# Kernel tuning notes

Hardware: AMD Instinct MI355X
Metric: run time of the kernel (lower is better)

## Reference

```python
import jax, jax.numpy as jnp
import numpy as np

N_NODES = 100000


def gcn_conv(x, src, dst, W, b, n):
    # PyG GCNConv: h = x @ W; add self-loops; sym-normalize; scatter-add; + bias
    h = x @ W                                        # [N, out]
    loop = jnp.arange(n, dtype=src.dtype)
    src2 = jnp.concatenate([src, loop])              # [E+N]
    dst2 = jnp.concatenate([dst, loop])
    deg = jax.ops.segment_sum(jnp.ones_like(dst2, dtype=h.dtype), dst2, num_segments=n)
    dis = jnp.where(deg > 0, jax.lax.rsqrt(deg), 0.0)
    norm = dis[src2] * dis[dst2]                     # [E+N]
    msg = h[src2] * norm[:, None]                    # gather + scale
    out = jax.ops.segment_sum(msg, dst2, num_segments=n)  # scatter-add
    return out + b


def setup_inputs() -> dict:
    key = jax.random.key(0)
    ks = jax.random.split(key, 8)
    F_in, H = 128, 64
    E = 1200000
    x = jax.random.normal(ks[0], (N_NODES, F_in), dtype=jnp.float32)
    edge_index = jax.random.randint(ks[1], (2, E), 0, N_NODES, dtype=jnp.int64)
    s = 1.0 / np.sqrt(F_in)
    W1 = jax.random.normal(ks[2], (F_in, H), dtype=jnp.float32) * s
    b1 = jnp.zeros((H,), dtype=jnp.float32)
    W2 = jax.random.normal(ks[3], (H, H), dtype=jnp.float32) * (1.0 / np.sqrt(H))
    b2 = jnp.zeros((H,), dtype=jnp.float32)
    W3 = jax.random.normal(ks[4], (H, 1), dtype=jnp.float32) * (1.0 / np.sqrt(H))
    b3 = jnp.zeros((1,), dtype=jnp.float32)
    return {"x": x, "edge_index": edge_index, "W1": W1, "b1": b1,
            "W2": W2, "b2": b2, "W3": W3, "b3": b3}


def reference(x, edge_index, W1, b1, W2, b2, W3, b3):
    n = x.shape[0]
    src, dst = edge_index[0], edge_index[1]
    h = jax.nn.relu(gcn_conv(x, src, dst, W1, b1, n))
    h = jax.nn.relu(gcn_conv(h, src, dst, W2, b2, n))
    return (h @ W3 + b3)[:, 0]  # squeeze(-1) -> [N]
```

## Files before the change

### kernel.cpp

```cpp
#include <hip/hip_runtime.h>

#define NF 64
#define NBKMAX 512
#define CHUNK 4096
#define CAP   4096

typedef __attribute__((ext_vector_type(8))) short bf16x8;
typedef __attribute__((ext_vector_type(4))) float f32x4;

__device__ __forceinline__ unsigned short f2bf(float f) {
    union { float f; unsigned u; } c; c.f = f;
    unsigned u = c.u;
    return (unsigned short)((u + 0x7FFFu + ((u >> 16) & 1u)) >> 16);
}
__device__ __forceinline__ float bf2f1(unsigned short v) {
    union { unsigned u; float f; } c; c.u = ((unsigned)v) << 16;
    return c.f;
}
__device__ __forceinline__ float2 bfp2(unsigned v) {
    union { unsigned u; float f; } lo, hi;
    lo.u = v << 16;
    hi.u = v & 0xffff0000u;
    return make_float2(lo.f, hi.f);
}

__global__ __launch_bounds__(256) void k_prep(int* __restrict__ bcnt, int nbk,
                                              const float* __restrict__ W1,
                                              unsigned short* __restrict__ wt1h,
                                              unsigned short* __restrict__ wt1l,
                                              const float* __restrict__ W2,
                                              unsigned short* __restrict__ wt2h,
                                              unsigned short* __restrict__ wt2l) {
    int idx = blockIdx.x * 256 + threadIdx.x;
    if (idx < 512) {
        if (idx < nbk) bcnt[idx] = 0;
    } else if (idx < 512 + 128 * 64) {
        int e = idx - 512;
        int k = e >> 6, col = e & 63;
        float w = W1[e];
        unsigned short h = f2bf(w);
        wt1h[col * 128 + k] = h;
        wt1l[col * 128 + k] = f2bf(w - bf2f1(h));
    } else if (idx < 512 + 128 * 64 + 64 * 64) {
        int e = idx - 512 - 128 * 64;
        int k = e >> 6, col = e & 63;
        float w = W2[e];
        unsigned short h = f2bf(w);
        wt2h[col * 64 + k] = h;
        wt2l[col * 64 + k] = f2bf(w - bf2f1(h));
    }
}

__device__ __forceinline__ void load8f(const float* A, bool ok, size_t off, float* v) {
    if (ok) {
        float4 a = *(const float4*)&A[off];
        float4 b = *(const float4*)&A[off + 4];
        v[0]=a.x; v[1]=a.y; v[2]=a.z; v[3]=a.w;
        v[4]=b.x; v[5]=b.y; v[6]=b.z; v[7]=b.w;
    } else { for (int j = 0; j < 8; ++j) v[j] = 0.f; }
}
__device__ __forceinline__ void load8f(const unsigned short* A, bool ok, size_t off, float* v) {
    if (ok) {
        uint4 u = *(const uint4*)&A[off];
        float2 p0 = bfp2(u.x), p1 = bfp2(u.y), p2 = bfp2(u.z), p3 = bfp2(u.w);
        v[0]=p0.x; v[1]=p0.y; v[2]=p1.x; v[3]=p1.y;
        v[4]=p2.x; v[5]=p2.y; v[6]=p3.x; v[7]=p3.y;
    } else { for (int j = 0; j < 8; ++j) v[j] = 0.f; }
}

template<int K>
__device__ __forceinline__ void stage_w(const unsigned short* __restrict__ Wt_hi_g,
                                        const unsigned short* __restrict__ Wt_lo_g,
                                        unsigned short* __restrict__ sWh,
                                        unsigned short* __restrict__ sWl, int tid) {
    constexpr int KS = K / 8, SM = KS - 1;
    for (int idx = tid; idx < 64 * KS; idx += 256) {
        int col = idx / KS, slot = idx % KS;
        int d = col * K + 8 * (slot ^ (col & SM));
        *(uint4*)&sWh[d] = *(const uint4*)&Wt_hi_g[col * K + slot * 8];
        *(uint4*)&sWl[d] = *(const uint4*)&Wt_lo_g[col * K + slot * 8];
    }
}

template<int K, bool HASBIAS, typename AT>
__device__ __forceinline__ void gemm_core(const AT* __restrict__ A,
                                          const unsigned short* __restrict__ sWh,
                                          const unsigned short* __restrict__ sWl,
                                          const float* __restrict__ bias_in,
                                          unsigned short* __restrict__ out,
                                          int n, int rb, int tid) {
    constexpr int KS = K / 8, SM = KS - 1, NS = K / 32;
    const int w = tid >> 6, l = tid & 63;
    const int lr = l & 15, lg = l >> 4;
    const int arow = rb + w * 16 + lr;
    const bool ok = arow < n;

    float v[NS][8];
    #pragma unroll
    for (int s = 0; s < NS; ++s)
        load8f(A, ok, (size_t)arow * K + s * 32 + lg * 8, v[s]);

    f32x4 acc[4] = {};
    #pragma unroll
    for (int s = 0; s < NS; ++s) {
        if (HASBIAS) {
            #pragma unroll
            for (int j = 0; j < 8; ++j)
                v[s][j] = fmaxf(v[s][j] + bias_in[s * 32 + lg * 8 + j], 0.f);
        }
        unsigned short h8[8], l8[8];
        #pragma unroll
        for (int j = 0; j < 8; ++j) {
            h8[j] = f2bf(v[s][j]);
            l8[j] = f2bf(v[s][j] - bf2f1(h8[j]));
        }
        const bf16x8 ah = *(const bf16x8*)h8;
        const bf16x8 al = *(const bf16x8*)l8;
        #pragma unroll
        for (int ct = 0; ct < 4; ++ct) {
            int col  = ct * 16 + lr;
            int boff = col * K + 8 * ((s * 4 + lg) ^ (col & SM));
            const bf16x8 bh = *(const bf16x8*)&sWh[boff];
            const bf16x8 bl = *(const bf16x8*)&sWl[boff];
            acc[ct] = __builtin_amdgcn_mfma_f32_16x16x32_bf16(ah, bh, acc[ct], 0, 0, 0);
            acc[ct] = __builtin_amdgcn_mfma_f32_16x16x32_bf16(ah, bl, acc[ct], 0, 0, 0);
            acc[ct] = __builtin_amdgcn_mfma_f32_16x16x32_bf16(al, bh, acc[ct], 0, 0, 0);
        }
    }

    #pragma unroll
    for (int i = 0; i < 4; ++i) {
        int r = rb + w * 16 + lg * 4 + i;
        if (r < n) {
            #pragma unroll
            for (int ct = 0; ct < 4; ++ct)
                out[(size_t)r * NF + ct * 16 + lr] = f2bf(acc[ct][i]);
        }
    }
}

struct ScatS {
    unsigned stage[CHUNK];
    unsigned short stb[CHUNK];
    int hist[NBKMAX];
    int base[NBKMAX];
};
struct GemmS {
    unsigned short sWh[64 * 128];
    unsigned short sWl[64 * 128];
};
union USmem { ScatS s; GemmS g; };

__global__ __launch_bounds__(256) void k_scat_gemm(
        const int* __restrict__ src, const int* __restrict__ dst,
        int* __restrict__ bcnt, unsigned* __restrict__ pairs4, int E, int nbk, int nscat,
        const float* __restrict__ A,
        const unsigned short* __restrict__ Wt_hi_g, const unsigned short* __restrict__ Wt_lo_g,
        unsigned short* __restrict__ out, int n) {
    __shared__ USmem u;
    const int tid = threadIdx.x;

    if ((int)blockIdx.x < nscat) {
        int e0 = blockIdx.x * CHUNK;
        int cnt = E - e0; if (cnt > CHUNK) cnt = CHUNK;
        for (int i = tid; i < nbk; i += 256) u.s.hist[i] = 0;
        __syncthreads();
        for (int i = tid; i < cnt; i += 256) {
            int s = src[e0 + i], d = dst[e0 + i];
            u.s.stage[i] = ((unsigned)s << 8) | ((unsigned)d & 255u);
            u.s.stb[i]   = (unsigned short)(((unsigned)d) >> 8);
            atomicAdd(&u.s.hist[((unsigned)d) >> 8], 1);
        }
        __syncthreads();
        for (int i = tid; i < nbk; i += 256) {
            int c = u.s.hist[i];
            u.s.base[i] = c ? atomicAdd(&bcnt[i], c) : 0;
            u.s.hist[i] = 0;
        }
        __syncthreads();
        for (int i = tid; i < cnt; i += 256) {
            int b = u.s.stb[i];
            int off = u.s.base[b] + atomicAdd(&u.s.hist[b], 1);
            if (off < CAP) pairs4[(size_t)b * CAP + off] = u.s.stage[i];
        }
        return;
    }

    const int rb = ((int)blockIdx.x - nscat) * 64;
    stage_w<128>(Wt_hi_g, Wt_lo_g, u.g.sWh, u.g.sWl, tid);
    __syncthreads();
    gemm_core<128, false>(A, u.g.sWh, u.g.sWl, nullptr, out, n, rb, tid);
}

__global__ __launch_bounds__(256) void k_bsort2(const unsigned* __restrict__ pairs4,
                                                const int* __restrict__ bcnt,
                                                int* __restrict__ start, int* __restrict__ endp,
                                                int* __restrict__ adj,
                                                float* __restrict__ dis, int n) {
    __shared__ int cnt[256];
    __shared__ int cur[256];
    int b   = blockIdx.x;
    int nb  = b << 8;
    int nn  = n - nb; if (nn > 256) nn = 256;
    int ec  = bcnt[b]; if (ec > CAP) ec = CAP;
    int pbI = b * CAP;
    size_t pb = (size_t)pbI;
    int t = threadIdx.x;
    cnt[t] = 0;
    __syncthreads();
    for (int i = t; i < ec; i += 256)
        atomicAdd(&cnt[pairs4[pb + i] & 255u], 1);
    __syncthreads();
    int v = cnt[t];
    __syncthreads();
    for (int off = 1; off < 256; off <<= 1) {
        int u = (t >= off) ? cnt[t - off] : 0;
        __syncthreads();
        cnt[t] += u;
        __syncthreads();
    }
    int exc = cnt[t] - v;
    if (t < nn) {
        start[nb + t] = pbI + exc;
        endp[nb + t]  = pbI + exc + v;
        dis[nb + t]   = rsqrtf((float)(v + 1));
    }
    cur[t] = exc;
    __syncthreads();
    for (int i = t; i < ec; i += 256) {
        unsigned p = pairs4[pb + i];
        int off = atomicAdd(&cur[p & 255u], 1);
        adj[pbI + off] = (int)(p >> 8);
    }
}

__global__ __launch_bounds__(256) void k_mgemm64(const unsigned short* __restrict__ A,
                                                 const unsigned short* __restrict__ Wt_hi_g,
                                                 const unsigned short* __restrict__ Wt_lo_g,
                                                 const float* __restrict__ bias_in,
                                                 unsigned short* __restrict__ out, int n) {
    __shared__ unsigned short sWh[64 * 64];
    __shared__ unsigned short sWl[64 * 64];
    const int tid = threadIdx.x;
    const int rb = blockIdx.x * 64;
    stage_w<64>(Wt_hi_g, Wt_lo_g, sWh, sWl, tid);
    __syncthreads();
    gemm_core<64, true>(A, sWh, sWl, bias_in, out, n, rb, tid);
}

__global__ __launch_bounds__(256) void k_gather(const unsigned short* __restrict__ g,
                                                const int* __restrict__ adj,
                                                const int* __restrict__ start,
                                                const int* __restrict__ endp,
                                                const float* __restrict__ dis,
                                                unsigned short* __restrict__ agg, int n) {
    int node = blockIdx.x * 16 + (threadIdx.x >> 4);
    int fl   = threadIdx.x & 15;
    int gb   = threadIdx.x & 48;
    if (node >= n) return;
    int s = start[node], e = endp[node];
    float dn = dis[node];
    uint2 v = *(const uint2*)&g[(size_t)node * NF + fl * 4];
    float2 pa = bfp2(v.x), pb = bfp2(v.y);
    float4 acc = make_float4(pa.x * dn, pa.y * dn, pb.x * dn, pb.y * dn);
    for (int base = s; base < e; base += 16) {
        int m = e - base; if (m > 16) m = 16;
        int idx = (fl < m) ? adj[base + fl] : 0;
        for (int j = 0; j < m; ++j) {
            int u = __shfl(idx, gb + j);
            float du = dis[u];
            uint2 w = *(const uint2*)&g[(size_t)u * NF + fl * 4];
            float2 q0 = bfp2(w.x), q1 = bfp2(w.y);
            acc.x += q0.x * du; acc.y += q0.y * du;
            acc.z += q1.x * du; acc.w += q1.y * du;
        }
    }
    ushort4 o;
    o.x = f2bf(acc.x * dn);
    o.y = f2bf(acc.y * dn);
    o.z = f2bf(acc.z * dn);
    o.w = f2bf(acc.w * dn);
    *(ushort4*)&agg[(size_t)node * NF + fl * 4] = o;
}

__global__ __launch_bounds__(256) void k_gather_final(const unsigned short* __restrict__ g,
                                                      const int* __restrict__ adj,
                                                      const int* __restrict__ start,
                                                      const int* __restrict__ endp,
                                                      const float* __restrict__ dis,
                                                      const float* __restrict__ b2,
                                                      const float* __restrict__ W3,
                                                      const float* __restrict__ b3,
                                                      float* __restrict__ out, int n) {
    int node = blockIdx.x * 16 + (threadIdx.x >> 4);
    int fl   = threadIdx.x & 15;
    int gb   = threadIdx.x & 48;
    if (node >= n) return;
    int s = start[node], e = endp[node];
    float dn = dis[node];
    uint2 v = *(const uint2*)&g[(size_t)node * NF + fl * 4];
    float2 pa = bfp2(v.x), pb = bfp2(v.y);
    float4 acc = make_float4(pa.x * dn, pa.y * dn, pb.x * dn, pb.y * dn);
    for (int base = s; base < e; base += 16) {
        int m = e - base; if (m > 16) m = 16;
        int idx = (fl < m) ? adj[base + fl] : 0;
        for (int j = 0; j < m; ++j) {
            int u = __shfl(idx, gb + j);
            float du = dis[u];
            uint2 w = *(const uint2*)&g[(size_t)u * NF + fl * 4];
            float2 q0 = bfp2(w.x), q1 = bfp2(w.y);
            acc.x += q0.x * du; acc.y += q0.y * du;
            acc.z += q1.x * du; acc.w += q1.y * du;
        }
    }
    const float4 bb = *(const float4*)&b2[fl * 4];
    const float4 ww = *(const float4*)&W3[fl * 4];
    float r = fmaxf(acc.x * dn + bb.x, 0.f) * ww.x
            + fmaxf(acc.y * dn + bb.y, 0.f) * ww.y
            + fmaxf(acc.z * dn + bb.z, 0.f) * ww.z
            + fmaxf(acc.w * dn + bb.w, 0.f) * ww.w;
    #pragma unroll
    for (int off = 8; off > 0; off >>= 1) r += __shfl_down(r, off, 16);
    if (fl == 0) out[node] = r + b3[0];
}

extern "C" void kernel_launch(void* const* d_in, const int* in_sizes, int n_in,
                              void* d_out, int out_size, void* d_ws, size_t ws_size,
                              hipStream_t stream) {
    const float* x  = (const float*)d_in[0];
    const int*   ei = (const int*)d_in[1];
    const float* W1 = (const float*)d_in[2];
    const float* b1 = (const float*)d_in[3];
    const float* W2 = (const float*)d_in[4];
    const float* b2 = (const float*)d_in[5];
    const float* W3 = (const float*)d_in[6];
    const float* b3 = (const float*)d_in[7];
    float* out = (float*)d_out;

    const int n = out_size;
    const int E = in_sizes[1] / 2;
    const int* src = ei;
    const int* dst = ei + E;
    const int ns  = (n + 255) & ~255;
    const int nbk = (n + 255) >> 8;

    char* w = (char*)d_ws;
    float* dis   = (float*)w;  w += (size_t)ns * 4;
    int*   start = (int*)w;    w += (size_t)ns * 4;
    int*   endp  = (int*)w;    w += (size_t)ns * 4;
    int*   adj   = (int*)w;    w += (size_t)nbk * CAP * 4;
    int*   bcnt  = (int*)w;    w += NBKMAX * 4;
    unsigned short* wt1h = (unsigned short*)w;  w += 64 * 128 * 2;
    unsigned short* wt1l = (unsigned short*)w;  w += 64 * 128 * 2;
    unsigned short* wt2h = (unsigned short*)w;  w += 64 * 64 * 2;
    unsigned short* wt2l = (unsigned short*)w;  w += 64 * 64 * 2;
    unsigned short* gbuf1 = (unsigned short*)w;  w += (size_t)n * NF * 2;
    unsigned short* gbuf2 = (unsigned short*)w;  w += (size_t)n * NF * 2;
    unsigned short* aggb  = (unsigned short*)w;  w += (size_t)n * NF * 2;
    unsigned* pairs4 = (unsigned*)w;

    const int B = 256;
    const int nscat = (E + CHUNK - 1) / CHUNK;
    const int ngemm = (n + 63) / 64;

    k_prep<<<(512 + 128 * 64 + 64 * 64 + B - 1) / B, B, 0, stream>>>(
        bcnt, nbk, W1, wt1h, wt1l, W2, wt2h, wt2l);
    k_scat_gemm<<<nscat + ngemm, B, 0, stream>>>(
        src, dst, bcnt, pairs4, E, nbk, nscat, x, wt1h, wt1l, gbuf1, n);
    k_bsort2<<<nbk, B, 0, stream>>>(pairs4, bcnt, start, endp, adj, dis, n);

    k_gather<<<(n + 15) / 16, B, 0, stream>>>(gbuf1, adj, start, endp, dis, aggb, n);

    k_mgemm64<<<ngemm, B, 0, stream>>>(aggb, wt2h, wt2l, b1, gbuf2, n);
    k_gather_final<<<(n + 15) / 16, B, 0, stream>>>(gbuf2, adj, start, endp, dis, b2, W3, b3, out, n);
}
```

Before: 128.4 us.

## Fuse layer-1 neighbor gather with layer-2 GEMM via shared memory

Merges the first-layer aggregation kernel and the second-layer 64x64 GEMM into one 1024-thread kernel. Each block gathers 64 nodes into fp32 shared memory, then applies bias, ReLU and the split-bf16 MFMA GEMM straight from LDS. This removes the aggb intermediate round trip through global memory and one kernel launch. In exchange, the large 1024-thread blocks may reduce occupancy and stall on the slowest node's gather, and the gathered values skip the bf16 rounding they had before.

Result: slower. 134.3 us (+4.6%).

```diff
diff --git a/kernel.cpp b/kernel.cpp
--- a/kernel.cpp
+++ b/kernel.cpp
@@ -59,83 +59,18 @@
         v[4]=b.x; v[5]=b.y; v[6]=b.z; v[7]=b.w;
     } else { for (int j = 0; j < 8; ++j) v[j] = 0.f; }
 }
-__device__ __forceinline__ void load8f(const unsigned short* A, bool ok, size_t off, float* v) {
-    if (ok) {
-        uint4 u = *(const uint4*)&A[off];
-        float2 p0 = bfp2(u.x), p1 = bfp2(u.y), p2 = bfp2(u.z), p3 = bfp2(u.w);
-        v[0]=p0.x; v[1]=p0.y; v[2]=p1.x; v[3]=p1.y;
-        v[4]=p2.x; v[5]=p2.y; v[6]=p3.x; v[7]=p3.y;
-    } else { for (int j = 0; j < 8; ++j) v[j] = 0.f; }
-}
 
 template<int K>
 __device__ __forceinline__ void stage_w(const unsigned short* __restrict__ Wt_hi_g,
                                         const unsigned short* __restrict__ Wt_lo_g,
                                         unsigned short* __restrict__ sWh,
-                                        unsigned short* __restrict__ sWl, int tid) {
+                                        unsigned short* __restrict__ sWl, int tid, int nthr) {
     constexpr int KS = K / 8, SM = KS - 1;
-    for (int idx = tid; idx < 64 * KS; idx += 256) {
+    for (int idx = tid; idx < 64 * KS; idx += nthr) {
         int col = idx / KS, slot = idx % KS;
         int d = col * K + 8 * (slot ^ (col & SM));
         *(uint4*)&sWh[d] = *(const uint4*)&Wt_hi_g[col * K + slot * 8];
         *(uint4*)&sWl[d] = *(const uint4*)&Wt_lo_g[col * K + slot * 8];
-    }
-}
-
-template<int K, bool HASBIAS, typename AT>
-__device__ __forceinline__ void gemm_core(const AT* __restrict__ A,
-                                          const unsigned short* __restrict__ sWh,
-                                          const unsigned short* __restrict__ sWl,
-                                          const float* __restrict__ bias_in,
-                                          unsigned short* __restrict__ out,
-                                          int n, int rb, int tid) {
-    constexpr int KS = K / 8, SM = KS - 1, NS = K / 32;
-    const int w = tid >> 6, l = tid & 63;
-    const int lr = l & 15, lg = l >> 4;
-    const int arow = rb + w * 16 + lr;
-    const bool ok = arow < n;
-
-    float v[NS][8];
-    #pragma unroll
-    for (int s = 0; s < NS; ++s)
-        load8f(A, ok, (size_t)arow * K + s * 32 + lg * 8, v[s]);
-
-    f32x4 acc[4] = {};
-    #pragma unroll
-    for (int s = 0; s < NS; ++s) {
-        if (HASBIAS) {
-            #pragma unroll
-            for (int j = 0; j < 8; ++j)
-                v[s][j] = fmaxf(v[s][j] + bias_in[s * 32 + lg * 8 + j], 0.f);
-        }
-        unsigned short h8[8], l8[8];
-        #pragma unroll
-        for (int j = 0; j < 8; ++j) {
-            h8[j] = f2bf(v[s][j]);
-            l8[j] = f2bf(v[s][j] - bf2f1(h8[j]));
-        }
-        const bf16x8 ah = *(const bf16x8*)h8;
-        const bf16x8 al = *(const bf16x8*)l8;
-        #pragma unroll
-        for (int ct = 0; ct < 4; ++ct) {
-            int col  = ct * 16 + lr;
-            int boff = col * K + 8 * ((s * 4 + lg) ^ (col & SM));
-            const bf16x8 bh = *(const bf16x8*)&sWh[boff];
-            const bf16x8 bl = *(const bf16x8*)&sWl[boff];
-            acc[ct] = __builtin_amdgcn_mfma_f32_16x16x32_bf16(ah, bh, acc[ct], 0, 0, 0);
-            acc[ct] = __builtin_amdgcn_mfma_f32_16x16x32_bf16(ah, bl, acc[ct], 0, 0, 0);
-            acc[ct] = __builtin_amdgcn_mfma_f32_16x16x32_bf16(al, bh, acc[ct], 0, 0, 0);
-        }
-    }
-
-    #pragma unroll
-    for (int i = 0; i < 4; ++i) {
-        int r = rb + w * 16 + lg * 4 + i;
-        if (r < n) {
-            #pragma unroll
-            for (int ct = 0; ct < 4; ++ct)
-                out[(size_t)r * NF + ct * 16 + lr] = f2bf(acc[ct][i]);
-        }
     }
 }
 
@@ -186,10 +121,53 @@
         return;
     }
 
+    constexpr int K = 128;
+    constexpr int KS = K / 8, SM = KS - 1, NS = K / 32;
     const int rb = ((int)blockIdx.x - nscat) * 64;
-    stage_w<128>(Wt_hi_g, Wt_lo_g, u.g.sWh, u.g.sWl, tid);
-    __syncthreads();
-    gemm_core<128, false>(A, u.g.sWh, u.g.sWl, nullptr, out, n, rb, tid);
+    stage_w<128>(Wt_hi_g, Wt_lo_g, u.g.sWh, u.g.sWl, tid, 256);
+    __syncthreads();
+
+    const int w = tid >> 6, l = tid & 63;
+    const int lr = l & 15, lg = l >> 4;
+    const int arow = rb + w * 16 + lr;
+    const bool ok = arow < n;
+
+    float v[NS][8];
+    #pragma unroll
+    for (int s = 0; s < NS; ++s)
+        load8f(A, ok, (size_t)arow * K + s * 32 + lg * 8, v[s]);
+
+    f32x4 acc[4] = {};
+    #pragma unroll
+    for (int s = 0; s < NS; ++s) {
+        unsigned short h8[8], l8[8];
+        #pragma unroll
+        for (int j = 0; j < 8; ++j) {
+            h8[j] = f2bf(v[s][j]);
+            l8[j] = f2bf(v[s][j] - bf2f1(h8[j]));
+        }
+        const bf16x8 ah = *(const bf16x8*)h8;
+        const bf16x8 al = *(const bf16x8*)l8;
+        #pragma unroll
+        for (int ct = 0; ct < 4; ++ct) {
+            int col  = ct * 16 + lr;
+            int boff = col * K + 8 * ((s * 4 + lg) ^ (col & SM));
+            const bf16x8 bh = *(const bf16x8*)&u.g.sWh[boff];
+            const bf16x8 bl = *(const bf16x8*)&u.g.sWl[boff];
+            acc[ct] = __builtin_amdgcn_mfma_f32_16x16x32_bf16(ah, bh, acc[ct], 0, 0, 0);
+            acc[ct] = __builtin_amdgcn_mfma_f32_16x16x32_bf16(ah, bl, acc[ct], 0, 0, 0);
+            acc[ct] = __builtin_amdgcn_mfma_f32_16x16x32_bf16(al, bh, acc[ct], 0, 0, 0);
+        }
+    }
+    #pragma unroll
+    for (int i = 0; i < 4; ++i) {
+        int r = rb + w * 16 + lg * 4 + i;
+        if (r < n) {
+            #pragma unroll
+            for (int ct = 0; ct < 4; ++ct)
+                out[(size_t)r * NF + ct * 16 + lr] = f2bf(acc[ct][i]);
+        }
+    }
 }
 
 __global__ __launch_bounds__(256) void k_bsort2(const unsigned* __restrict__ pairs4,
@@ -234,53 +212,91 @@
     }
 }
 
-__global__ __launch_bounds__(256) void k_mgemm64(const unsigned short* __restrict__ A,
-                                                 const unsigned short* __restrict__ Wt_hi_g,
-                                                 const unsigned short* __restrict__ Wt_lo_g,
-                                                 const float* __restrict__ bias_in,
-                                                 unsigned short* __restrict__ out, int n) {
+__global__ __launch_bounds__(1024) void k_gather_gemm(
+        const unsigned short* __restrict__ g,
+        const int* __restrict__ adj, const int* __restrict__ start,
+        const int* __restrict__ endp, const float* __restrict__ dis,
+        const unsigned short* __restrict__ wt2h_g, const unsigned short* __restrict__ wt2l_g,
+        const float* __restrict__ b1,
+        unsigned short* __restrict__ out, int n) {
+    __shared__ float sA[64 * 64];
     __shared__ unsigned short sWh[64 * 64];
     __shared__ unsigned short sWl[64 * 64];
     const int tid = threadIdx.x;
     const int rb = blockIdx.x * 64;
-    stage_w<64>(Wt_hi_g, Wt_lo_g, sWh, sWl, tid);
-    __syncthreads();
-    gemm_core<64, true>(A, sWh, sWl, bias_in, out, n, rb, tid);
-}
-
-__global__ __launch_bounds__(256) void k_gather(const unsigned short* __restrict__ g,
-                                                const int* __restrict__ adj,
-                                                const int* __restrict__ start,
-                                                const int* __restrict__ endp,
-                                                const float* __restrict__ dis,
-                                                unsigned short* __restrict__ agg, int n) {
-    int node = blockIdx.x * 16 + (threadIdx.x >> 4);
-    int fl   = threadIdx.x & 15;
-    int gb   = threadIdx.x & 48;
-    if (node >= n) return;
-    int s = start[node], e = endp[node];
-    float dn = dis[node];
-    uint2 v = *(const uint2*)&g[(size_t)node * NF + fl * 4];
-    float2 pa = bfp2(v.x), pb = bfp2(v.y);
-    float4 acc = make_float4(pa.x * dn, pa.y * dn, pb.x * dn, pb.y * dn);
-    for (int base = s; base < e; base += 16) {
-        int m = e - base; if (m > 16) m = 16;
-        int idx = (fl < m) ? adj[base + fl] : 0;
-        for (int j = 0; j < m; ++j) {
-            int u = __shfl(idx, gb + j);
-            float du = dis[u];
-            uint2 w = *(const uint2*)&g[(size_t)u * NF + fl * 4];
-            float2 q0 = bfp2(w.x), q1 = bfp2(w.y);
-            acc.x += q0.x * du; acc.y += q0.y * du;
-            acc.z += q1.x * du; acc.w += q1.y * du;
-        }
-    }
-    ushort4 o;
-    o.x = f2bf(acc.x * dn);
-    o.y = f2bf(acc.y * dn);
-    o.z = f2bf(acc.z * dn);
-    o.w = f2bf(acc.w * dn);
-    *(ushort4*)&agg[(size_t)node * NF + fl * 4] = o;
+
+    stage_w<64>(wt2h_g, wt2l_g, sWh, sWl, tid, 1024);
+
+    {
+        int local = tid >> 4;
+        int node  = rb + local;
+        int fl = tid & 15;
+        int gb = tid & 48;
+        float4 acc = make_float4(0.f, 0.f, 0.f, 0.f);
+        if (node < n) {
+            int s = start[node], e = endp[node];
+            float dn = dis[node];
+            uint2 v = *(const uint2*)&g[(size_t)node * NF + fl * 4];
+            float2 pa = bfp2(v.x), pb = bfp2(v.y);
+            acc = make_float4(pa.x * dn, pa.y * dn, pb.x * dn, pb.y * dn);
+            for (int base = s; base < e; base += 16) {
+                int m = e - base; if (m > 16) m = 16;
+                int idx = (fl < m) ? adj[base + fl] : 0;
+                for (int j = 0; j < m; ++j) {
+                    int u = __shfl(idx, gb + j);
+                    float du = dis[u];
+                    uint2 w = *(const uint2*)&g[(size_t)u * NF + fl * 4];
+                    float2 q0 = bfp2(w.x), q1 = bfp2(w.y);
+                    acc.x += q0.x * du; acc.y += q0.y * du;
+                    acc.z += q1.x * du; acc.w += q1.y * du;
+                }
+            }
+            acc.x *= dn; acc.y *= dn; acc.z *= dn; acc.w *= dn;
+        }
+        int d = local * 64 + 4 * (fl ^ (local & 15));
+        *(float4*)&sA[d] = acc;
+    }
+    __syncthreads();
+
+    const int w = tid >> 6, l = tid & 63;
+    const int lr = l & 15, lg = l >> 4;
+    const int rg = (w & 3) * 16 + lr;
+    const int ct = w >> 2;
+    f32x4 a4 = {};
+    #pragma unroll
+    for (int s = 0; s < 2; ++s) {
+        float v8[8];
+        #pragma unroll
+        for (int half = 0; half < 2; ++half) {
+            int slot = s * 8 + lg * 2 + half;
+            int d = rg * 64 + 4 * (slot ^ (rg & 15));
+            float4 t = *(const float4*)&sA[d];
+            v8[half * 4 + 0] = t.x; v8[half * 4 + 1] = t.y;
+            v8[half * 4 + 2] = t.z; v8[half * 4 + 3] = t.w;
+        }
+        unsigned short h8[8], l8[8];
+        #pragma unroll
+        for (int j = 0; j < 8; ++j) {
+            float vv = fmaxf(v8[j] + b1[s * 32 + lg * 8 + j], 0.f);
+            h8[j] = f2bf(vv);
+            l8[j] = f2bf(vv - bf2f1(h8[j]));
+        }
+        const bf16x8 ah = *(const bf16x8*)h8;
+        const bf16x8 al = *(const bf16x8*)l8;
+        int col  = ct * 16 + lr;
+        int boff = col * 64 + 8 * ((s * 4 + lg) ^ (col & 7));
+        const bf16x8 bh = *(const bf16x8*)&sWh[boff];
+        const bf16x8 bl = *(const bf16x8*)&sWl[boff];
+        a4 = __builtin_amdgcn_mfma_f32_16x16x32_bf16(ah, bh, a4, 0, 0, 0);
+        a4 = __builtin_amdgcn_mfma_f32_16x16x32_bf16(ah, bl, a4, 0, 0, 0);
+        a4 = __builtin_amdgcn_mfma_f32_16x16x32_bf16(al, bh, a4, 0, 0, 0);
+    }
+    #pragma unroll
+    for (int i = 0; i < 4; ++i) {
+        int r = rb + (w & 3) * 16 + lg * 4 + i;
+        if (r < n)
+            out[(size_t)r * NF + ct * 16 + lr] = f2bf(a4[i]);
+    }
 }
 
 __global__ __launch_bounds__(256) void k_gather_final(const unsigned short* __restrict__ g,
@@ -356,7 +372,6 @@
     unsigned short* wt2l = (unsigned short*)w;  w += 64 * 64 * 2;
     unsigned short* gbuf1 = (unsigned short*)w;  w += (size_t)n * NF * 2;
     unsigned short* gbuf2 = (unsigned short*)w;  w += (size_t)n * NF * 2;
-    unsigned short* aggb  = (unsigned short*)w;  w += (size_t)n * NF * 2;
     unsigned* pairs4 = (unsigned*)w;
 
     const int B = 256;
@@ -369,8 +384,8 @@
         src, dst, bcnt, pairs4, E, nbk, nscat, x, wt1h, wt1l, gbuf1, n);
     k_bsort2<<<nbk, B, 0, stream>>>(pairs4, bcnt, start, endp, adj, dis, n);
 
-    k_gather<<<(n + 15) / 16, B, 0, stream>>>(gbuf1, adj, start, endp, dis, aggb, n);
-
-    k_mgemm64<<<ngemm, B, 0, stream>>>(aggb, wt2h, wt2l, b1, gbuf2, n);
+    k_gather_gemm<<<ngemm, 1024, 0, stream>>>(
+        gbuf1, adj, start, endp, dis, wt2h, wt2l, b1, gbuf2, n);
+
     k_gather_final<<<(n + 15) / 16, B, 0, stream>>>(gbuf2, adj, start, endp, dis, b2, W3, b3, out, n);
 }
```
